# Kernel tuning notes

Measured on AMD Instinct MI355X. Metric: run time of the kernel, lower is better.

The kernel has to match this reference:

```python
import jax, jax.numpy as jnp
import numpy as np


def conv(x, w, groups=1):
    # x: NCHW, w: OIHW, stride 1, SAME padding
    return jax.lax.conv_general_dilated(
        x, w, (1, 1), 'SAME', feature_group_count=groups,
        dimension_numbers=('NCHW', 'OIHW', 'NCHW'))


def bn(x, scale, shift):
    # eval-mode BatchNorm folded into per-channel affine
    return x * scale[None, :, None, None] + shift[None, :, None, None]


def ghost_expert(x, Wp, sp, bp, Wc, sc, bc, out_ch):
    # primary conv 3x3 (C_in -> init_ch) + BN + SiLU
    x1 = jax.nn.silu(bn(conv(x, Wp), sp, bp))
    # cheap depthwise 3x3 (groups = init_ch) + BN + SiLU
    x2 = jax.nn.silu(bn(conv(x1, Wc, groups=x1.shape[1]), sc, bc))
    return jnp.concatenate([x1, x2], axis=1)[:, :out_ch]


def setup_inputs() -> dict:
    key = jax.random.key(0)
    ks = jax.random.split(key, 20)
    B, Cin, Cout, H, W = 8, 256, 256, 64, 64
    E, red, init_ch, new_ch = 4, 32, 128, 128
    f = lambda k, shape, s=0.05: jax.random.normal(k, shape, jnp.float32) * s
    g = lambda k, shape: jax.random.uniform(k, shape, jnp.float32, 0.5, 1.5)
    inp = dict(
        x=jax.random.normal(ks[0], (B, Cin, H, W), jnp.float32),
        # router: conv3x3 Cin->red, BN, SiLU, conv1x1 red->E, BN
        Wr1=f(ks[1], (red, Cin, 3, 3)), sr1=g(ks[2], (red,)), br1=f(ks[3], (red,), 0.1),
        Wr2=f(ks[4], (E, red, 1, 1)), sr2=g(ks[5], (E,)), br2=f(ks[6], (E,), 0.1),
        # E ghost experts (stacked on leading expert axis)
        We_p=f(ks[7], (E, init_ch, Cin, 3, 3)), se_p=g(ks[8], (E, init_ch)), be_p=f(ks[9], (E, init_ch), 0.1),
        We_c=f(ks[10], (E, new_ch, 1, 3, 3)), se_c=g(ks[11], (E, new_ch)), be_c=f(ks[12], (E, new_ch), 0.1),
        # shared ghost expert
        Ws_p=f(ks[13], (init_ch, Cin, 3, 3)), ss_p=g(ks[14], (init_ch,)), bs_p=f(ks[15], (init_ch,), 0.1),
        Ws_c=f(ks[16], (new_ch, 1, 3, 3)), ss_c=g(ks[17], (new_ch,)), bs_c=f(ks[18], (new_ch,), 0.1),
        top_k=2,
    )
    return inp


def reference(x, Wr1, sr1, br1, Wr2, sr2, br2,
              We_p, se_p, be_p, We_c, se_c, be_c,
              Ws_p, ss_p, bs_p, Ws_c, ss_c, bs_c, top_k):
    B, Cin, H, W = x.shape
    E = Wr2.shape[0]
    Cout = 256
    pool_scale = 4
    # ---- EfficientSpatialRouter (eval mode: no noise) ----
    xd = x.reshape(B, Cin, H // pool_scale, pool_scale, W // pool_scale, pool_scale).mean((3, 5))
    h = jax.nn.silu(bn(conv(xd, Wr1), sr1, br1))
    logits = bn(conv(h, Wr2), sr2, br2)           # [B, E, H/4, W/4]
    global_logits = logits.mean(axis=(2, 3))      # [B, E]
    weights = jax.nn.softmax(global_logits, axis=1)
    topk_vals, topk_idx = jax.lax.top_k(weights, top_k)
    topk_vals = topk_vals / (topk_vals.sum(axis=1, keepdims=True) + 1e-6)
    # ---- dense all-expert compute + weighted combine ----
    run = lambda Wp, sp, bp, Wc, sc, bc: ghost_expert(x, Wp, sp, bp, Wc, sc, bc, Cout)
    expert_outs = jax.vmap(run)(We_p, se_p, be_p, We_c, se_c, be_c)  # [E,B,Cout,H,W]
    w_full = (topk_vals[:, :, None] * jax.nn.one_hot(topk_idx, E, dtype=x.dtype)).sum(1)  # [B,E]
    combined = jnp.einsum('be,ebchw->bchw', w_full, expert_outs)
    # ---- shared expert for stability ----
    shared = ghost_expert(x, Ws_p, ss_p, bs_p, Ws_c, ss_c, bs_c, Cout)
    return combined + shared
```

## Files before the change

### kernel.cpp

```cpp
#include <hip/hip_runtime.h>
#include <hip/hip_bf16.h>

constexpr int BATCH = 8;
constexpr int CIN   = 256;
constexpr int HH    = 64;
constexpr int WW    = 64;
constexpr int NPIX  = HH * WW;
constexpr int ICH   = 128;

constexpr size_t OFF_XD    = 0;
constexpr size_t OFF_HMEAN = 524288;
constexpr size_t OFF_WFULL = 524544;
constexpr size_t OFF_SLOT  = 524608;
constexpr size_t OFF_WTB   = 524672;
constexpr size_t OFF_XBP   = OFF_WTB + 737280;
constexpr size_t OFF_X1B   = OFF_XBP + 4460544;

typedef __bf16  bf16x8 __attribute__((ext_vector_type(8)));
typedef float   f32x4  __attribute__((ext_vector_type(4)));

__device__ __forceinline__ float silu_f(float v) { return v / (1.f + __expf(-v)); }

__device__ __forceinline__ unsigned short f2bf(float f) {
    return __builtin_bit_cast(unsigned short, __float2bfloat16(f));
}
__device__ __forceinline__ float bf2f(unsigned short u) {
    return __builtin_bit_cast(float, (unsigned)u << 16);
}
__device__ __forceinline__ bf16x8 ld_frag(const ushort* p) {
    uint4 v = *(const uint4*)p;
    return __builtin_bit_cast(bf16x8, v);
}
__device__ __forceinline__ void gload16(const ushort* g, ushort* l) {
    __builtin_amdgcn_global_load_lds(
        (const __attribute__((address_space(1))) void*)g,
        (__attribute__((address_space(3))) void*)l, 16, 0, 0);
}

__global__ void k_avgpool(const float* __restrict__ x, float* __restrict__ xd)
{
    int t = blockIdx.x * 256 + threadIdx.x;
    int jb = t & 3, i = (t >> 2) & 15, c = (t >> 6) & 255, b = t >> 14;
    const float* src = x + ((size_t)(b * CIN + c) * HH + i * 4) * WW + jb * 16;
    float s0 = 0.f, s1 = 0.f, s2 = 0.f, s3 = 0.f;
#pragma unroll
    for (int r = 0; r < 4; ++r) {
        const float4* p = (const float4*)(src + r * WW);
        float4 a = p[0], b4 = p[1], c4 = p[2], d4 = p[3];
        s0 += a.x + a.y + a.z + a.w;
        s1 += b4.x + b4.y + b4.z + b4.w;
        s2 += c4.x + c4.y + c4.z + c4.w;
        s3 += d4.x + d4.y + d4.z + d4.w;
    }
    float4 o;
    o.x = s0 * 0.0625f; o.y = s1 * 0.0625f; o.z = s2 * 0.0625f; o.w = s3 * 0.0625f;
    *(float4*)(xd + ((size_t)(b * CIN + c) * 16 + i) * 16 + jb * 4) = o;
}

__global__ __launch_bounds__(256) void k_xprep(const float* __restrict__ x,
                                               ushort* __restrict__ xbp)
{
    int b = blockIdx.x >> 6, row = blockIdx.x & 63;
    __shared__ ushort tile[64 * 258];
    int tid = threadIdx.x;
    const float* src = x + ((size_t)b * CIN * HH + row) * WW;
    for (int k = tid; k < 256 * 64; k += 256) {
        int cin = k >> 6, col = k & 63;
        tile[col * 258 + cin] = f2bf(src[(size_t)cin * NPIX + col]);
    }
    __syncthreads();
    ushort* dst = xbp + ((size_t)(b * 66 + row + 1) * 66 + 1) * 256;
    for (int k = tid; k < 64 * 128; k += 256) {
        int col = k >> 7, cp = (k & 127) * 2;
        unsigned u0 = tile[col * 258 + cp];
        unsigned u1 = tile[col * 258 + cp + 1];
        *(unsigned*)(dst + (size_t)col * 256 + cp) = u0 | (u1 << 16);
    }
}

__global__ __launch_bounds__(256) void k_router_conv(
    const float* __restrict__ xd, const float* __restrict__ Wr1,
    const float* __restrict__ sr1, const float* __restrict__ br1,
    float* __restrict__ hmean)
{
    int b = blockIdx.x >> 5, r = blockIdx.x & 31;
    __shared__ float wl[9 * 256];
    __shared__ float red[256];
    int tid = threadIdx.x;
    for (int k = tid; k < 2304; k += 256) {
        int cin = k / 9, tap = k % 9;
        wl[tap * 256 + cin] = Wr1[r * 2304 + k];
    }
    __syncthreads();
    const float* xb = xd + (size_t)b * CIN * 256;
    int i = tid >> 4, j = tid & 15;
    float acc = 0.f;
#pragma unroll
    for (int kh = 0; kh < 3; ++kh) {
        int ii = i + kh - 1;
        bool oki = (unsigned)ii < 16u;
        int iis = oki ? ii : 0;
#pragma unroll
        for (int kw = 0; kw < 3; ++kw) {
            int jj = j + kw - 1;
            bool ok = oki && ((unsigned)jj < 16u);
            int off = iis * 16 + (((unsigned)jj < 16u) ? jj : 0);
            const float* wt = wl + (kh * 3 + kw) * 256;
            float t = 0.f;
#pragma unroll 8
            for (int cin = 0; cin < 256; ++cin)
                t = fmaf(wt[cin], xb[cin * 256 + off], t);
            if (ok) acc += t;
        }
    }
    float h = silu_f(acc * sr1[r] + br1[r]);
    red[tid] = h;
    __syncthreads();
    for (int st = 128; st > 0; st >>= 1) {
        if (tid < st) red[tid] += red[tid + st];
        __syncthreads();
    }
    if (tid == 0) hmean[b * 32 + r] = red[0] * (1.f / 256.f);
}

__global__ void k_router_final(const float* __restrict__ hmean,
                               const float* __restrict__ Wr2, const float* __restrict__ sr2,
                               const float* __restrict__ br2, const int* __restrict__ topk_p,
                               float* __restrict__ wfull, int* __restrict__ slot)
{
    __shared__ float lg[8][4];
    __shared__ float wf[8][5];
    int tid = threadIdx.x;
    if (tid < 32) {
        int b = tid >> 2, e = tid & 3;
        float a = 0.f;
        for (int r = 0; r < 32; ++r) a += Wr2[e * 32 + r] * hmean[b * 32 + r];
        lg[b][e] = a * sr2[e] + br2[e];
    }
    __syncthreads();
    if (tid < 8) {
        int b = tid;
        float l0 = lg[b][0], l1 = lg[b][1], l2 = lg[b][2], l3 = lg[b][3];
        float mx = fmaxf(fmaxf(l0, l1), fmaxf(l2, l3));
        float e0 = __expf(l0 - mx), e1 = __expf(l1 - mx), e2 = __expf(l2 - mx), e3 = __expf(l3 - mx);
        float sum = e0 + e1 + e2 + e3;
        float w[4] = { e0 / sum, e1 / sum, e2 / sum, e3 / sum };
        int k = topk_p[0];
        if (k > 4) k = 4;
        bool taken[4] = { false, false, false, false };
        float tv[4]; int ti[4]; float tsum = 0.f;
        for (int t = 0; t < k; ++t) {
            float best = -1e30f; int bi = 0;
            for (int e = 0; e < 4; ++e)
                if (!taken[e] && w[e] > best) { best = w[e]; bi = e; }
            taken[bi] = true; tv[t] = best; ti[t] = bi; tsum += best;
        }
        float inv = 1.f / (tsum + 1e-6f);
        float o[4] = { 0.f, 0.f, 0.f, 0.f };
        for (int t = 0; t < k; ++t) o[ti[t]] = tv[t] * inv;
        for (int e = 0; e < 4; ++e) { wf[b][e] = o[e]; wfull[b * 5 + e] = o[e]; }
        wf[b][4] = 1.f; wfull[b * 5 + 4] = 1.f;
    }
    __syncthreads();
    if (tid == 0) {
        int cnt = 0;
        for (int s = 0; s < 5; ++s)
            for (int b = 0; b < 8; ++b)
                slot[s * 8 + b] = (wf[b][s] != 0.f) ? (cnt++) : -1;
    }
}

__global__ void k_wprep16(const float* __restrict__ We_p, const float* __restrict__ Ws_p,
                          ushort* __restrict__ wtb)
{
    int t = blockIdx.x * 256 + threadIdx.x;
    int k5  = t & 31;
    int oc  = (t >> 5) & 63;
    int tap = (t >> 11) % 9;
    int blk = t / 18432;
    int chunk = blk & 7;
    int h     = (blk >> 3) & 1;
    int s     = blk >> 4;
    int cin   = chunk * 32 + k5;
    int ocg   = h * 64 + oc;
    float v = (s < 4) ? We_p[((size_t)(s * 128 + ocg) * 256 + cin) * 9 + tap]
                      : Ws_p[((size_t)ocg * 256 + cin) * 9 + tap];
    wtb[t] = f2bf(v);
}

__global__ __launch_bounds__(256, 1) void k_primary_mfma(
    const ushort* __restrict__ xbp, const ushort* __restrict__ wtb,
    const float* __restrict__ se_p, const float* __restrict__ be_p,
    const float* __restrict__ ss_p, const float* __restrict__ bs_p,
    const int* __restrict__ slot, ushort* __restrict__ x1b)
{
    int pass = blockIdx.y;
    int sl = slot[pass];
    if (sl < 0) return;
    int s = pass >> 3, b = pass & 7;
    int och = blockIdx.x >> 4;
    int tile = blockIdx.x & 15;
    int row0 = (tile >> 2) * 16, col0 = (tile & 3) * 16;

    __shared__ ushort wlds[2][2304 * 8];
    __shared__ ushort xlds[2][1344 * 8];

    int tid = threadIdx.x;
    int wv = tid >> 6, lane = tid & 63;
    int ks = lane >> 4, c = lane & 15;

    const ushort* xb_b = xbp + (size_t)b * 66 * 66 * 256;
    const ushort* wslab = wtb + (size_t)(s * 2 + och) * (8 * 18432);

    int goff[6];
#pragma unroll
    for (int it = 0; it < 5; ++it) {
        int k = it * 256 + tid;
        int r = k / 72, rem = k % 72, ks2 = rem / 18, c2 = rem % 18;
        goff[it] = ((row0 + r) * 66 + (col0 + c2)) * 256 + ks2 * 8;
    }
    {
        int k = 1280 + lane;
        int r = k / 72, rem = k % 72, ks2 = rem / 18, c2 = rem % 18;
        goff[5] = ((row0 + r) * 66 + (col0 + c2)) * 256 + ks2 * 8;
    }
    int lds_us = wv * 512;

    f32x4 acc[4][4];
#pragma unroll
    for (int m = 0; m < 4; ++m)
#pragma unroll
        for (int n = 0; n < 4; ++n) acc[m][n] = (f32x4){0.f, 0.f, 0.f, 0.f};

    int Sb = 4 * wv * 72 + ks * 18 + c;

    auto stage = [&](int ch, int buf) {
        const ushort* wsrc = wslab + ch * 18432;
#pragma unroll
        for (int it = 0; it < 9; ++it)
            gload16(wsrc + (size_t)(it * 256 + tid) * 8,
                    &wlds[buf][(size_t)(it * 2048 + lds_us)]);
        const ushort* xsrc = xb_b + ch * 32;
#pragma unroll
        for (int it = 0; it < 5; ++it)
            gload16(xsrc + goff[it], &xlds[buf][(size_t)(it * 2048 + lds_us)]);
        if (wv == 0) gload16(xsrc + goff[5], &xlds[buf][1280 * 8]);
    };

    stage(0, 0);
    __syncthreads();

    int cur = 0;
    for (int ch = 0; ch < 8; ++ch) {
        if (ch < 7) stage(ch + 1, cur ^ 1);
        const ushort* wl = &wlds[cur][0];
        const ushort* xl = &xlds[cur][0];
#pragma unroll
        for (int kh = 0; kh < 3; ++kh) {
#pragma unroll
            for (int kw = 0; kw < 3; ++kw) {
                int tap = kh * 3 + kw;
                bf16x8 afr[4];
#pragma unroll
                for (int m = 0; m < 4; ++m)
                    afr[m] = ld_frag(wl + ((size_t)(tap * 64 + m * 16 + c) * 4 + ks) * 8);
#pragma unroll
                for (int n = 0; n < 4; ++n) {
                    bf16x8 bfr = ld_frag(xl + (size_t)(Sb + (n + kh) * 72 + kw) * 8);
#pragma unroll
                    for (int m = 0; m < 4; ++m)
                        acc[m][n] = __builtin_amdgcn_mfma_f32_16x16x32_bf16(
                            afr[m], bfr, acc[m][n], 0, 0, 0);
                }
            }
        }
        __syncthreads();
        cur ^= 1;
    }

    const float* scale = (s < 4) ? (se_p + s * ICH) : ss_p;
    const float* shift = (s < 4) ? (be_p + s * ICH) : bs_p;
    ushort* outp = x1b + (size_t)sl * (ICH * NPIX);
    int colg = col0 + c;
#pragma unroll
    for (int m = 0; m < 4; ++m) {
#pragma unroll
        for (int n = 0; n < 4; ++n) {
            int rowg = row0 + 4 * wv + n;
#pragma unroll
            for (int j = 0; j < 4; ++j) {
                int oc = och * 64 + m * 16 + ks * 4 + j;
                float v = acc[m][n][j] * scale[oc] + shift[oc];
                outp[(size_t)oc * NPIX + rowg * 64 + colg] = f2bf(silu_f(v));
            }
        }
    }
}

__global__ __launch_bounds__(256) void k_cheap(
    const ushort* __restrict__ x1b, const float* __restrict__ We_c,
    const float* __restrict__ se_c, const float* __restrict__ be_c,
    const float* __restrict__ Ws_c, const float* __restrict__ ss_c,
    const float* __restrict__ bs_c, const float* __restrict__ wfull,
    const int* __restrict__ slot, float* __restrict__ out)
{
    int blk = blockIdx.x;
    int b = blk >> 7, c = blk & 127;
    __shared__ float img[3][66][66];
    int tid = threadIdx.x;

    int nact = 0;
    int sls[3], sidx[3];
    float wgts[3];
    for (int s = 0; s < 5; ++s) {
        int sl = slot[s * 8 + b];
        if (sl < 0) continue;
        sls[nact] = sl; sidx[nact] = s;
        wgts[nact] = (s < 4) ? wfull[b * 5 + s] : 1.0f;
        ++nact;
    }

    for (int k = tid; k < 3 * 66 * 66; k += 256) ((float*)img)[k] = 0.f;
    __syncthreads();

#pragma unroll
    for (int a = 0; a < 3; ++a) {
        if (a < nact) {
            const ushort* src = x1b + ((size_t)sls[a] * ICH + c) * NPIX;
            for (int k = tid; k < 1024; k += 256) {
                int i = k >> 4, jc = (k & 15) * 4;
                uint2 u = *(const uint2*)(src + i * 64 + jc);
                img[a][1 + i][1 + jc] = bf2f((unsigned short)(u.x & 0xFFFFu));
                img[a][1 + i][2 + jc] = bf2f((unsigned short)(u.x >> 16));
                img[a][1 + i][3 + jc] = bf2f((unsigned short)(u.y & 0xFFFFu));
                img[a][1 + i][4 + jc] = bf2f((unsigned short)(u.y >> 16));
            }
        }
    }
    __syncthreads();

    float o1[16], o2[16];
#pragma unroll
    for (int t = 0; t < 16; ++t) { o1[t] = 0.f; o2[t] = 0.f; }

#pragma unroll
    for (int a = 0; a < 3; ++a) {
        if (a < nact) {
            int s = sidx[a];
            const float* wp = (s < 4) ? (We_c + (size_t)(s * ICH + c) * 9)
                                      : (Ws_c + (size_t)c * 9);
            float wc0 = wp[0], wc1 = wp[1], wc2 = wp[2], wc3 = wp[3], wc4 = wp[4],
                  wc5 = wp[5], wc6 = wp[6], wc7 = wp[7], wc8 = wp[8];
            float sc = (s < 4) ? se_c[s * ICH + c] : ss_c[c];
            float sh = (s < 4) ? be_c[s * ICH + c] : bs_c[c];
            float wgt = wgts[a];
#pragma unroll
            for (int t = 0; t < 16; ++t) {
                int p = tid + t * 256;
                int i = p >> 6, j = p & 63;
                float center = img[a][1 + i][1 + j];
                float d = wc0 * img[a][i][j];
                d = fmaf(wc1, img[a][i][j + 1], d);
                d = fmaf(wc2, img[a][i][j + 2], d);
                d = fmaf(wc3, img[a][i + 1][j], d);
                d = fmaf(wc4, center, d);
                d = fmaf(wc5, img[a][i + 1][j + 2], d);
                d = fmaf(wc6, img[a][i + 2][j], d);
                d = fmaf(wc7, img[a][i + 2][j + 1], d);
                d = fmaf(wc8, img[a][i + 2][j + 2], d);
                float v = d * sc + sh;
                o1[t] += wgt * center;
                o2[t] += wgt * silu_f(v);
            }
        }
    }

    float* out1 = out + ((size_t)(b * 256) + c) * NPIX;
    float* out2 = out + ((size_t)(b * 256) + 128 + c) * NPIX;
#pragma unroll
    for (int t = 0; t < 16; ++t) {
        int p = tid + t * 256;
        out1[p] = o1[t];
        out2[p] = o2[t];
    }
}

extern "C" void kernel_launch(void* const* d_in, const int* in_sizes, int n_in,
                              void* d_out, int out_size, void* d_ws, size_t ws_size,
                              hipStream_t stream)
{
    const float* x    = (const float*)d_in[0];
    const float* Wr1  = (const float*)d_in[1];
    const float* sr1  = (const float*)d_in[2];
    const float* br1  = (const float*)d_in[3];
    const float* Wr2  = (const float*)d_in[4];
    const float* sr2  = (const float*)d_in[5];
    const float* br2  = (const float*)d_in[6];
    const float* We_p = (const float*)d_in[7];
    const float* se_p = (const float*)d_in[8];
    const float* be_p = (const float*)d_in[9];
    const float* We_c = (const float*)d_in[10];
    const float* se_c = (const float*)d_in[11];
    const float* be_c = (const float*)d_in[12];
    const float* Ws_p = (const float*)d_in[13];
    const float* ss_p = (const float*)d_in[14];
    const float* bs_p = (const float*)d_in[15];
    const float* Ws_c = (const float*)d_in[16];
    const float* ss_c = (const float*)d_in[17];
    const float* bs_c = (const float*)d_in[18];
    const int*  topk  = (const int*)d_in[19];
    float* out = (float*)d_out;
    float* ws  = (float*)d_ws;

    float*  xd    = ws + OFF_XD;
    float*  hmean = ws + OFF_HMEAN;
    float*  wfull = ws + OFF_WFULL;
    int*    slot  = (int*)(ws + OFF_SLOT);
    ushort* wtb   = (ushort*)(ws + OFF_WTB);
    ushort* xbp   = (ushort*)(ws + OFF_XBP);
    ushort* x1b   = (ushort*)(ws + OFF_X1B);

    hipMemsetAsync(xbp, 0, (size_t)8 * 66 * 66 * 256 * sizeof(ushort), stream);
    k_avgpool<<<512, 256, 0, stream>>>(x, xd);
    k_xprep<<<512, 256, 0, stream>>>(x, xbp);
    k_wprep16<<<5760, 256, 0, stream>>>(We_p, Ws_p, wtb);
    k_router_conv<<<256, 256, 0, stream>>>(xd, Wr1, sr1, br1, hmean);
    k_router_final<<<1, 64, 0, stream>>>(hmean, Wr2, sr2, br2, topk, wfull, slot);
    k_primary_mfma<<<dim3(32, 40), 256, 0, stream>>>(xbp, wtb, se_p, be_p, ss_p, bs_p, slot, x1b);
    k_cheap<<<1024, 256, 0, stream>>>(x1b, We_c, se_c, be_c, Ws_c, ss_c, bs_c, wfull, slot, out);
}
```

Before: 301.9 us.

## Triple-buffer input tiles with vmcnt-based barriers and reorder weight layout

The primary MFMA conv kernel now keeps input tiles in three LDS buffers and prefetches two chunks ahead. Each per-chunk __syncthreads is replaced by a partial s_waitcnt vmcnt plus s_barrier, so later loads can stay in flight. The weight prep kernel and the fragment load are changed to a ks-major, oc-contiguous layout, which gives contiguous LDS reads across lanes. The cost is more LDS use and delicate vmcnt counting that depends on how many loads each stage issues; all threads now issue the 6th x load, with padding offsets of zero.

```diff
diff --git a/kernel.cpp b/kernel.cpp
--- a/kernel.cpp
+++ b/kernel.cpp
@@ -174,14 +174,15 @@
                           ushort* __restrict__ wtb)
 {
     int t = blockIdx.x * 256 + threadIdx.x;
-    int k5  = t & 31;
-    int oc  = (t >> 5) & 63;
+    int j   = t & 7;
+    int oc  = (t >> 3) & 63;
+    int ks  = (t >> 9) & 3;
     int tap = (t >> 11) % 9;
     int blk = t / 18432;
     int chunk = blk & 7;
     int h     = (blk >> 3) & 1;
     int s     = blk >> 4;
-    int cin   = chunk * 32 + k5;
+    int cin   = chunk * 32 + ks * 8 + j;
     int ocg   = h * 64 + oc;
     float v = (s < 4) ? We_p[((size_t)(s * 128 + ocg) * 256 + cin) * 9 + tap]
                       : Ws_p[((size_t)ocg * 256 + cin) * 9 + tap];
@@ -203,7 +204,7 @@
     int row0 = (tile >> 2) * 16, col0 = (tile & 3) * 16;
 
     __shared__ ushort wlds[2][2304 * 8];
-    __shared__ ushort xlds[2][1344 * 8];
+    __shared__ ushort xlds[3][1536 * 8];
 
     int tid = threadIdx.x;
     int wv = tid >> 6, lane = tid & 63;
@@ -214,15 +215,14 @@
 
     int goff[6];
 #pragma unroll
-    for (int it = 0; it < 5; ++it) {
+    for (int it = 0; it < 6; ++it) {
         int k = it * 256 + tid;
-        int r = k / 72, rem = k % 72, ks2 = rem / 18, c2 = rem % 18;
-        goff[it] = ((row0 + r) * 66 + (col0 + c2)) * 256 + ks2 * 8;
-    }
-    {
-        int k = 1280 + lane;
-        int r = k / 72, rem = k % 72, ks2 = rem / 18, c2 = rem % 18;
-        goff[5] = ((row0 + r) * 66 + (col0 + c2)) * 256 + ks2 * 8;
+        if (k < 1296) {
+            int r = k / 72, rem = k % 72, ks2 = rem / 18, c2 = rem % 18;
+            goff[it] = ((row0 + r) * 66 + (col0 + c2)) * 256 + ks2 * 8;
+        } else {
+            goff[it] = 0;
+        }
     }
     int lds_us = wv * 512;
 
@@ -234,27 +234,39 @@
 
     int Sb = 4 * wv * 72 + ks * 18 + c;
 
-    auto stage = [&](int ch, int buf) {
-        const ushort* wsrc = wslab + ch * 18432;
-#pragma unroll
-        for (int it = 0; it < 9; ++it)
-            gload16(wsrc + (size_t)(it * 256 + tid) * 8,
-                    &wlds[buf][(size_t)(it * 2048 + lds_us)]);
-        const ushort* xsrc = xb_b + ch * 32;
-#pragma unroll
-        for (int it = 0; it < 5; ++it)
-            gload16(xsrc + goff[it], &xlds[buf][(size_t)(it * 2048 + lds_us)]);
-        if (wv == 0) gload16(xsrc + goff[5], &xlds[buf][1280 * 8]);
-    };
-
-    stage(0, 0);
-    __syncthreads();
-
-    int cur = 0;
+#define STAGE_W(ch, buf)                                                        \
+    {                                                                           \
+        const ushort* wsrc_ = wslab + (ch) * 18432;                             \
+        _Pragma("unroll")                                                       \
+        for (int it = 0; it < 9; ++it)                                          \
+            gload16(wsrc_ + (size_t)(it * 256 + tid) * 8,                       \
+                    &wlds[buf][(size_t)(it * 2048 + lds_us)]);                  \
+    }
+#define STAGE_X(ch, buf)                                                        \
+    {                                                                           \
+        const ushort* xsrc_ = xb_b + (ch) * 32;                                 \
+        _Pragma("unroll")                                                       \
+        for (int it = 0; it < 6; ++it)                                          \
+            gload16(xsrc_ + goff[it], &xlds[buf][(size_t)(it * 2048 + lds_us)]);\
+    }
+#define PIPE_BARRIER(N)                                                         \
+    asm volatile("s_waitcnt vmcnt(" #N ")" ::: "memory");                       \
+    __builtin_amdgcn_sched_barrier(0);                                          \
+    __builtin_amdgcn_s_barrier();                                               \
+    __builtin_amdgcn_sched_barrier(0);
+
+    STAGE_W(0, 0);
+    STAGE_X(0, 0);
+    STAGE_X(1, 1);
+    PIPE_BARRIER(6)
+
+    int wcur = 0;
     for (int ch = 0; ch < 8; ++ch) {
-        if (ch < 7) stage(ch + 1, cur ^ 1);
-        const ushort* wl = &wlds[cur][0];
-        const ushort* xl = &xlds[cur][0];
+        if (ch < 7) STAGE_W(ch + 1, wcur ^ 1);
+        if (ch < 6) STAGE_X(ch + 2, (ch + 2) % 3);
+
+        const ushort* wl = &wlds[wcur][0];
+        const ushort* xl = &xlds[ch % 3][0];
 #pragma unroll
         for (int kh = 0; kh < 3; ++kh) {
 #pragma unroll
@@ -263,7 +275,7 @@
                 bf16x8 afr[4];
 #pragma unroll
                 for (int m = 0; m < 4; ++m)
-                    afr[m] = ld_frag(wl + ((size_t)(tap * 64 + m * 16 + c) * 4 + ks) * 8);
+                    afr[m] = ld_frag(wl + ((size_t)((tap * 4 + ks) * 64) + m * 16 + c) * 8);
 #pragma unroll
                 for (int n = 0; n < 4; ++n) {
                     bf16x8 bfr = ld_frag(xl + (size_t)(Sb + (n + kh) * 72 + kw) * 8);
@@ -274,9 +286,16 @@
                 }
             }
         }
-        __syncthreads();
-        cur ^= 1;
-    }
+        if (ch < 6) {
+            PIPE_BARRIER(6)
+        } else if (ch == 6) {
+            PIPE_BARRIER(0)
+        }
+        wcur ^= 1;
+    }
+#undef STAGE_W
+#undef STAGE_X
+#undef PIPE_BARRIER
 
     const float* scale = (s < 4) ? (se_p + s * ICH) : ss_p;
     const float* shift = (s < 4) ? (be_p + s * ICH) : bs_p;
```

After: 300.9 us. About the same (-0.3%).

## Switch primary conv to 32x32x16 MFMA with larger 512-thread tiles

Applied to the files above, without the earlier changes.

Rewrites the primary 3x3 conv MFMA kernel to use 32x32x16 bf16 MFMA instead of 16x16x32. Each block now has 8 waves covering a 16x32 pixel tile, and the input-channel chunk shrinks from 32 to 16, so the K loop runs 16 steps. The weight pre-pack layout is changed to match. A raw waitcnt plus s_barrier pipeline replaces __syncthreads, and launch bounds allow two blocks per CU. The aim is fewer fragment LDS loads per FLOP and better occupancy. The risks are more barrier steps, half-filled third load groups, and register pressure from the 16-wide accumulators.

```diff
diff --git a/kernel.cpp b/kernel.cpp
--- a/kernel.cpp
+++ b/kernel.cpp
@@ -18,6 +18,7 @@
 
 typedef __bf16  bf16x8 __attribute__((ext_vector_type(8)));
 typedef float   f32x4  __attribute__((ext_vector_type(4)));
+typedef float   f32x16 __attribute__((ext_vector_type(16)));
 
 __device__ __forceinline__ float silu_f(float v) { return v / (1.f + __expf(-v)); }
 
@@ -174,21 +175,22 @@
                           ushort* __restrict__ wtb)
 {
     int t = blockIdx.x * 256 + threadIdx.x;
-    int k5  = t & 31;
-    int oc  = (t >> 5) & 63;
-    int tap = (t >> 11) % 9;
-    int blk = t / 18432;
-    int chunk = blk & 7;
-    int h     = (blk >> 3) & 1;
-    int s     = blk >> 4;
-    int cin   = chunk * 32 + k5;
-    int ocg   = h * 64 + oc;
+    int j    = t & 7;
+    int oc   = (t >> 3) & 63;
+    int ks2  = (t >> 9) & 1;
+    int tap  = (t >> 10) % 9;
+    int q    = t / 9216;
+    int chunk = q & 15;
+    int och   = (q >> 4) & 1;
+    int s     = q >> 5;
+    int cin   = chunk * 16 + ks2 * 8 + j;
+    int ocg   = och * 64 + oc;
     float v = (s < 4) ? We_p[((size_t)(s * 128 + ocg) * 256 + cin) * 9 + tap]
                       : Ws_p[((size_t)ocg * 256 + cin) * 9 + tap];
     wtb[t] = f2bf(v);
 }
 
-__global__ __launch_bounds__(256, 1) void k_primary_mfma(
+__global__ __launch_bounds__(512, 2) void k_primary_mfma(
     const ushort* __restrict__ xbp, const ushort* __restrict__ wtb,
     const float* __restrict__ se_p, const float* __restrict__ be_p,
     const float* __restrict__ ss_p, const float* __restrict__ bs_p,
@@ -198,99 +200,107 @@
     int sl = slot[pass];
     if (sl < 0) return;
     int s = pass >> 3, b = pass & 7;
-    int och = blockIdx.x >> 4;
-    int tile = blockIdx.x & 15;
-    int row0 = (tile >> 2) * 16, col0 = (tile & 3) * 16;
-
-    __shared__ ushort wlds[2][2304 * 8];
-    __shared__ ushort xlds[2][1344 * 8];
+    int och = blockIdx.x >> 3;
+    int pxt = blockIdx.x & 7;
+    int row0 = (pxt >> 1) * 16, col0 = (pxt & 1) * 32;
+
+    __shared__ ushort wbuf[2][1152 * 8];
+    __shared__ ushort xbuf[2][1224 * 8];
 
     int tid = threadIdx.x;
     int wv = tid >> 6, lane = tid & 63;
-    int ks = lane >> 4, c = lane & 15;
-
-    const ushort* xb_b = xbp + (size_t)b * 66 * 66 * 256;
-    const ushort* wslab = wtb + (size_t)(s * 2 + och) * (8 * 18432);
-
-    int goff[6];
-#pragma unroll
-    for (int it = 0; it < 5; ++it) {
-        int k = it * 256 + tid;
-        int r = k / 72, rem = k % 72, ks2 = rem / 18, c2 = rem % 18;
-        goff[it] = ((row0 + r) * 66 + (col0 + c2)) * 256 + ks2 * 8;
-    }
-    {
-        int k = 1280 + lane;
-        int r = k / 72, rem = k % 72, ks2 = rem / 18, c2 = rem % 18;
-        goff[5] = ((row0 + r) * 66 + (col0 + c2)) * 256 + ks2 * 8;
-    }
-    int lds_us = wv * 512;
-
-    f32x4 acc[4][4];
-#pragma unroll
-    for (int m = 0; m < 4; ++m)
-#pragma unroll
-        for (int n = 0; n < 4; ++n) acc[m][n] = (f32x4){0.f, 0.f, 0.f, 0.f};
-
-    int Sb = 4 * wv * 72 + ks * 18 + c;
-
-    auto stage = [&](int ch, int buf) {
-        const ushort* wsrc = wslab + ch * 18432;
-#pragma unroll
-        for (int it = 0; it < 9; ++it)
-            gload16(wsrc + (size_t)(it * 256 + tid) * 8,
-                    &wlds[buf][(size_t)(it * 2048 + lds_us)]);
-        const ushort* xsrc = xb_b + ch * 32;
-#pragma unroll
-        for (int it = 0; it < 5; ++it)
-            gload16(xsrc + goff[it], &xlds[buf][(size_t)(it * 2048 + lds_us)]);
-        if (wv == 0) gload16(xsrc + goff[5], &xlds[buf][1280 * 8]);
-    };
-
-    stage(0, 0);
-    __syncthreads();
-
-    int cur = 0;
-    for (int ch = 0; ch < 8; ++ch) {
-        if (ch < 7) stage(ch + 1, cur ^ 1);
-        const ushort* wl = &wlds[cur][0];
-        const ushort* xl = &xlds[cur][0];
+    int wr = wv >> 1, wc = wv & 1;
+    int l31 = lane & 31, ks2l = lane >> 5;
+    int r2 = (lane >> 4) & 1, c2 = lane & 15;
+
+    const ushort* xslab = xbp + (size_t)b * 66 * 66 * 256;
+    const ushort* wslab = wtb + (size_t)(s * 2 + och) * 147456;
+
+    int woff[3], wldb[3], xoff[3], xldb[3];
+#pragma unroll
+    for (int it = 0; it < 3; ++it) {
+        int wg = wv * 144 + it * 64 + lane;
+        if (wg > 1151) wg = 1151;
+        woff[it] = wg * 8;
+        wldb[it] = (wv * 144 + it * 64) * 8;
+        int g = wv * 153 + it * 64 + lane;
+        if (g > 1223) g = 1223;
+        int row = g / 68, rem = g % 68;
+        int k2 = rem / 34, col = rem % 34;
+        xoff[it] = ((row0 + row) * 66 + (col0 + col)) * 256 + k2 * 8;
+        xldb[it] = (wv * 153 + it * 64) * 8;
+    }
+
+    f32x16 acc[2][2];
+#pragma unroll
+    for (int mt = 0; mt < 2; ++mt)
+#pragma unroll
+        for (int nt = 0; nt < 2; ++nt)
+#pragma unroll
+            for (int r = 0; r < 16; ++r) acc[mt][nt][r] = 0.f;
+
+#define STAGE(ch, bf)                                                           \
+    {                                                                           \
+        const ushort* ws_ = wslab + (size_t)(ch) * 9216;                        \
+        gload16(ws_ + woff[0], &wbuf[bf][wldb[0]]);                             \
+        gload16(ws_ + woff[1], &wbuf[bf][wldb[1]]);                             \
+        if (lane < 16) gload16(ws_ + woff[2], &wbuf[bf][wldb[2]]);              \
+        const ushort* xs_ = xslab + (ch) * 16;                                  \
+        gload16(xs_ + xoff[0], &xbuf[bf][xldb[0]]);                             \
+        gload16(xs_ + xoff[1], &xbuf[bf][xldb[1]]);                             \
+        if (lane < 25) gload16(xs_ + xoff[2], &xbuf[bf][xldb[2]]);              \
+    }
+#define PIPE_BARRIER(N)                                                         \
+    asm volatile("s_waitcnt vmcnt(" #N ")" ::: "memory");                       \
+    __builtin_amdgcn_sched_barrier(0);                                          \
+    __builtin_amdgcn_s_barrier();                                               \
+    __builtin_amdgcn_sched_barrier(0);
+
+    STAGE(0, 0)
+    PIPE_BARRIER(0)
+
+    for (int ch = 0; ch < 16; ++ch) {
+        int cur = ch & 1;
+        if (ch < 15) STAGE(ch + 1, cur ^ 1)
+        const ushort* wl = &wbuf[cur][0];
+        const ushort* xl = &xbuf[cur][0];
 #pragma unroll
         for (int kh = 0; kh < 3; ++kh) {
 #pragma unroll
             for (int kw = 0; kw < 3; ++kw) {
                 int tap = kh * 3 + kw;
-                bf16x8 afr[4];
-#pragma unroll
-                for (int m = 0; m < 4; ++m)
-                    afr[m] = ld_frag(wl + ((size_t)(tap * 64 + m * 16 + c) * 4 + ks) * 8);
-#pragma unroll
-                for (int n = 0; n < 4; ++n) {
-                    bf16x8 bfr = ld_frag(xl + (size_t)(Sb + (n + kh) * 72 + kw) * 8);
-#pragma unroll
-                    for (int m = 0; m < 4; ++m)
-                        acc[m][n] = __builtin_amdgcn_mfma_f32_16x16x32_bf16(
-                            afr[m], bfr, acc[m][n], 0, 0, 0);
+                bf16x8 a0 = ld_frag(wl + (size_t)((tap * 2 + ks2l) * 64 + l31) * 8);
+                bf16x8 a1 = ld_frag(wl + (size_t)((tap * 2 + ks2l) * 64 + 32 + l31) * 8);
+#pragma unroll
+                for (int nt = 0; nt < 2; ++nt) {
+                    int row = wr * 4 + nt * 2 + r2 + kh;
+                    bf16x8 bf = ld_frag(xl + (size_t)(row * 68 + ks2l * 34 +
+                                                      wc * 16 + c2 + kw) * 8);
+                    acc[0][nt] = __builtin_amdgcn_mfma_f32_32x32x16_bf16(
+                        a0, bf, acc[0][nt], 0, 0, 0);
+                    acc[1][nt] = __builtin_amdgcn_mfma_f32_32x32x16_bf16(
+                        a1, bf, acc[1][nt], 0, 0, 0);
                 }
             }
         }
-        __syncthreads();
-        cur ^= 1;
-    }
+        if (ch < 15) PIPE_BARRIER(0)
+    }
+#undef STAGE
+#undef PIPE_BARRIER
 
     const float* scale = (s < 4) ? (se_p + s * ICH) : ss_p;
     const float* shift = (s < 4) ? (be_p + s * ICH) : bs_p;
     ushort* outp = x1b + (size_t)sl * (ICH * NPIX);
-    int colg = col0 + c;
-#pragma unroll
-    for (int m = 0; m < 4; ++m) {
-#pragma unroll
-        for (int n = 0; n < 4; ++n) {
-            int rowg = row0 + 4 * wv + n;
-#pragma unroll
-            for (int j = 0; j < 4; ++j) {
-                int oc = och * 64 + m * 16 + ks * 4 + j;
-                float v = acc[m][n][j] * scale[oc] + shift[oc];
+    int colg = col0 + wc * 16 + c2;
+#pragma unroll
+    for (int mt = 0; mt < 2; ++mt) {
+#pragma unroll
+        for (int nt = 0; nt < 2; ++nt) {
+            int rowg = row0 + wr * 4 + nt * 2 + r2;
+#pragma unroll
+            for (int r = 0; r < 16; ++r) {
+                int oc = och * 64 + mt * 32 + (r & 3) + 8 * (r >> 2) + 4 * ks2l;
+                float v = acc[mt][nt][r] * scale[oc] + shift[oc];
                 outp[(size_t)oc * NPIX + rowg * 64 + colg] = f2bf(silu_f(v));
             }
         }
@@ -426,6 +436,6 @@
     k_wprep16<<<5760, 256, 0, stream>>>(We_p, Ws_p, wtb);
     k_router_conv<<<256, 256, 0, stream>>>(xd, Wr1, sr1, br1, hmean);
     k_router_final<<<1, 64, 0, stream>>>(hmean, Wr2, sr2, br2, topk, wfull, slot);
-    k_primary_mfma<<<dim3(32, 40), 256, 0, stream>>>(xbp, wtb, se_p, be_p, ss_p, bs_p, slot, x1b);
+    k_primary_mfma<<<dim3(16, 40), 512, 0, stream>>>(xbp, wtb, se_p, be_p, ss_p, bs_p, slot, x1b);
     k_cheap<<<1024, 256, 0, stream>>>(x1b, We_c, se_c, be_c, Ws_c, ss_c, bs_c, wfull, slot, out);
 }
```

After: 306.7 us. No clear change (+1.6%).
